# Kernel optimization log

Measured on AMD Instinct MI355X. Metric: run time of the kernel, lower is better.

## Reference

```python
import jax, jax.numpy as jnp
import numpy as np

N_FIL, N_SUB = 13, 4
N_NODES = N_FIL * N_SUB  # 52
FEAT = 6
HID = 128
N_LAYERS = 3
BATCH = 4096


def build_microtubule_edges(nf=N_FIL, ns=N_SUB):
    edges = []
    for i in range(nf):
        for j in range(ns - 1):
            a = i * ns + j
            b = a + 1
            edges += [[a, b], [b, a]]
    for i in range(nf):
        for j in range(ns):
            a = i * ns + j
            l = ((i - 1) % nf) * ns + j
            edges += [[a, l], [l, a]]
            r = ((i + 1) % nf) * ns + j
            edges += [[a, r], [r, a]]
    return np.asarray(edges, dtype=np.int64).T  # (2, 286)


def setup_inputs() -> dict:
    key = jax.random.key(0)
    ks = jax.random.split(key, 10)
    inp = {
        "q_current": jax.random.normal(ks[0], (BATCH, N_FIL, N_SUB, FEAT), jnp.float32),
        "W_in": jax.random.normal(ks[1], (HID, FEAT), jnp.float32) * 0.3,
        "b_in": jax.random.normal(ks[2], (HID,), jnp.float32) * 0.02,
        "W_gnn": jax.random.normal(ks[3], (N_LAYERS, HID, HID), jnp.float32) * (1.0 / np.sqrt(HID)),
        "b_gnn": jax.random.normal(ks[4], (N_LAYERS, HID), jnp.float32) * 0.02,
        "W_d1": jax.random.normal(ks[5], (HID, HID), jnp.float32) * (1.0 / np.sqrt(HID)),
        "b_d1": jax.random.normal(ks[6], (HID,), jnp.float32) * 0.02,
        "W_d2": jax.random.normal(ks[7], (FEAT, HID), jnp.float32) * (1.0 / np.sqrt(HID)),
        "b_d2": jax.random.normal(ks[8], (FEAT,), jnp.float32) * 0.02,
        "edge_index": jnp.asarray(build_microtubule_edges()),
    }
    return inp


def reference(q_current, W_in, b_in, W_gnn, b_gnn, W_d1, b_d1, W_d2, b_d2, edge_index):
    B = q_current.shape[0]
    x0 = q_current.reshape(B, N_NODES, FEAT)

    # PyG GCNConv default: add self-loops, symmetric normalization.
    loops = jnp.arange(N_NODES, dtype=edge_index.dtype)
    src = jnp.concatenate([edge_index[0], loops])  # message source j
    dst = jnp.concatenate([edge_index[1], loops])  # aggregation target i
    deg = jax.ops.segment_sum(jnp.ones_like(dst, dtype=x0.dtype), dst,
                              num_segments=N_NODES)
    dinv = jax.lax.rsqrt(deg)  # deg >= 1 because of self-loops
    norm = (dinv[src] * dinv[dst])[None, :, None]  # (1, E, 1)

    # encoder (batched over B and nodes)
    x = jax.nn.relu(jnp.einsum('bnf,hf->bnh', x0, W_in) + b_in)

    for l in range(N_LAYERS):
        h = jnp.einsum('bnh,oh->bno', x, W_gnn[l])     # linear, no bias
        msg = h[:, src, :] * norm                      # gather + scale
        agg = jnp.zeros_like(h).at[:, dst, :].add(msg)  # scatter-add
        x = x + jax.nn.relu(agg + b_gnn[l])            # bias after agg, residual

    # decoder (Dropout is identity in eval)
    y = jax.nn.relu(jnp.einsum('bnh,oh->bno', x, W_d1) + b_d1)
    y = jnp.einsum('bnh,fh->bnf', y, W_d2) + b_d2
    return y.reshape(B, N_FIL, N_SUB, FEAT)
```

## Files before the change

kernel.cpp:

```cpp
#include <hip/hip_runtime.h>


typedef __attribute__((ext_vector_type(2)))  float  f32x2;
typedef __attribute__((ext_vector_type(4)))  float  f32x4;
typedef __attribute__((ext_vector_type(16))) float  f32x16;
typedef __attribute__((ext_vector_type(8)))  __bf16 bf16x8;

#define MFMA(a, b, c) __builtin_amdgcn_mfma_f32_32x32x16_bf16((a), (b), (c), 0, 0, 0)

__device__ __forceinline__ int xidx(int row, int kdw) {
    return row * 128 + (kdw ^ ((row & 7) << 2));
}

struct bfpair { __bf16 h, l; };
__device__ __forceinline__ bfpair splitf(float f) {
    bfpair p;
    p.h = (__bf16)f;
    p.l = (__bf16)(f - (float)p.h);
    return p;
}

__global__ __launch_bounds__(256) void prep_w(
    const float* __restrict__ Wg, const float* __restrict__ Wd1,
    __bf16* __restrict__ ws)
{
    const int tid  = blockIdx.x * 256 + threadIdx.x;
    const int lane = tid & 31;
    const int hi   = (tid >> 5) & 1;
    const int ot   = (tid >> 6) & 3;
    const int kc   = (tid >> 8) & 7;
    const int L    = tid >> 11;
    const float* src = ((L < 3) ? (Wg + L * 16384) : Wd1)
                     + (ot * 32 + lane) * 128 + kc * 16 + hi * 8;
    const f32x4 v0 = *(const f32x4*)(src);
    const f32x4 v1 = *(const f32x4*)(src + 4);
    bf16x8 h8, l8;
    #pragma unroll
    for (int e = 0; e < 4; ++e) {
        bfpair p0 = splitf(v0[e]); h8[e]   = p0.h; l8[e]   = p0.l;
        bfpair p1 = splitf(v1[e]); h8[4+e] = p1.h; l8[4+e] = p1.l;
    }
    ((bf16x8*)ws)[tid]        = h8;
    ((bf16x8*)ws)[8192 + tid] = l8;
}

__global__ __launch_bounds__(128, 3) void mt_fwd(
    const float* __restrict__ q,   const float* __restrict__ Win, const float* __restrict__ bin,
    const float* __restrict__ bg,  const float* __restrict__ bd1,
    const float* __restrict__ Wd2, const float* __restrict__ bd2,
    const bf16x8* __restrict__ Ph, float* __restrict__ out)
{
    __shared__ __attribute__((aligned(16))) float xs[52 * 128];

    const int t    = threadIdx.x;
    const int nt   = t >> 6;
    const int l    = t & 63;
    const int lane = l & 31;
    const int hi   = l >> 5;
    const int n    = nt * 32 + lane;
    const int nc   = (n < 52) ? n : 0;
    const int samp = blockIdx.x;
    const bf16x8* Pl = Ph + 8192;

    int nb[5]; float nw[5];
    {
        const int   fi = n >> 2, js = n & 3;
        const float dg = 5.f + (js > 0 ? 1.f : 0.f) + (js < 3 ? 1.f : 0.f);
        const float di = rsqrtf(dg);
        nb[0] = n;                          nw[0] = di * di;
        nb[1] = ((fi + 12) % 13) * 4 + js;  nw[1] = 2.f * di * di;
        nb[2] = ((fi + 1) % 13) * 4 + js;   nw[2] = 2.f * di * di;
        nb[3] = (js > 0) ? (n - 1) : 0;
        nw[3] = (js > 0) ? di * rsqrtf(6.f + (js > 1 ? 1.f : 0.f)) : 0.f;
        nb[4] = (js < 3) ? (n + 1) : 0;
        nw[4] = (js < 3) ? di * rsqrtf(6.f + (js < 2 ? 1.f : 0.f)) : 0.f;
        if (n >= 52) {
            #pragma unroll
            for (int c = 0; c < 5; ++c) { nb[c] = 0; nw[c] = 0.f; }
        }
    }

    {
        f32x4 z4; z4[0]=0.f; z4[1]=0.f; z4[2]=0.f; z4[3]=0.f;
        f32x4 u0 = z4, u1 = z4;
        if (hi == 0 && n < 52) {
            const float* qp = q + (samp * 52 + n) * 6;
            const f32x2 a = *(const f32x2*)(qp);
            const f32x2 b = *(const f32x2*)(qp + 2);
            const f32x2 c = *(const f32x2*)(qp + 4);
            u0[0]=a[0]; u0[1]=a[1]; u0[2]=b[0]; u0[3]=b[1]; u1[0]=c[0]; u1[1]=c[1];
        }
        bf16x8 bh, bl;
        #pragma unroll
        for (int e = 0; e < 4; ++e) {
            bfpair p0 = splitf(u0[e]); bh[e]   = p0.h; bl[e]   = p0.l;
            bfpair p1 = splitf(u1[e]); bh[4+e] = p1.h; bl[4+e] = p1.l;
        }

        #pragma unroll
        for (int ot = 0; ot < 4; ++ot) {
            f32x4 v0 = z4, v1 = z4;
            if (hi == 0) {
                const int o_r = ot * 32 + lane;
                const f32x2 a = *(const f32x2*)(Win + o_r * 6);
                const f32x2 b = *(const f32x2*)(Win + o_r * 6 + 2);
                const f32x2 c = *(const f32x2*)(Win + o_r * 6 + 4);
                v0[0]=a[0]; v0[1]=a[1]; v0[2]=b[0]; v0[3]=b[1]; v1[0]=c[0]; v1[1]=c[1];
            }
            bf16x8 ah, al;
            #pragma unroll
            for (int e = 0; e < 4; ++e) {
                bfpair p0 = splitf(v0[e]); ah[e]   = p0.h; al[e]   = p0.l;
                bfpair p1 = splitf(v1[e]); ah[4+e] = p1.h; al[4+e] = p1.l;
            }
            f32x16 acc;
            #pragma unroll
            for (int r = 0; r < 16; ++r) acc[r] = 0.f;
            acc = MFMA(ah, bh, acc);
            acc = MFMA(ah, bl, acc);
            acc = MFMA(al, bh, acc);
            if (n < 52) {
                #pragma unroll
                for (int j = 0; j < 4; ++j) {
                    const f32x4 bv = *(const f32x4*)(bin + ot * 32 + 8 * j + 4 * hi);
                    f32x4 v;
                    #pragma unroll
                    for (int e = 0; e < 4; ++e) v[e] = fmaxf(acc[4 * j + e] + bv[e], 0.f);
                    *(f32x4*)&xs[xidx(n, ot * 32 + 8 * j + 4 * hi)] = v;
                }
            }
        }
    }

    #pragma unroll 1
    for (int L = 0; L < 4; ++L) {
        __syncthreads();

        f32x16 acc[4];
        #pragma unroll
        for (int ot = 0; ot < 4; ++ot)
            #pragma unroll
            for (int r = 0; r < 16; ++r) acc[ot][r] = 0.f;

        const int fbase = (L * 8) * 256;

        #pragma unroll 1
        for (int kc = 0; kc < 8; ++kc) {
            const int kb = kc * 16 + 8 * hi;
            f32x4 a0, a1;
            if (L < 3) {
                #pragma unroll
                for (int e = 0; e < 4; ++e) { a0[e] = 0.f; a1[e] = 0.f; }
                #pragma unroll
                for (int c = 0; c < 5; ++c) {
                    const f32x4 x0 = *(const f32x4*)&xs[xidx(nb[c], kb)];
                    const f32x4 x1 = *(const f32x4*)&xs[xidx(nb[c], kb + 4)];
                    a0 += nw[c] * x0;
                    a1 += nw[c] * x1;
                }
            } else {
                a0 = *(const f32x4*)&xs[xidx(nc, kb)];
                a1 = *(const f32x4*)&xs[xidx(nc, kb + 4)];
            }
            bf16x8 bh, bl;
            #pragma unroll
            for (int e = 0; e < 4; ++e) {
                bfpair p0 = splitf(a0[e]); bh[e]   = p0.h; bl[e]   = p0.l;
                bfpair p1 = splitf(a1[e]); bh[4+e] = p1.h; bl[4+e] = p1.l;
            }

            const int fk = fbase + kc * 256 + hi * 32 + lane;
            #pragma unroll
            for (int ot = 0; ot < 4; ++ot) {
                const bf16x8 wh = Ph[fk + ot * 64];
                const bf16x8 wl = Pl[fk + ot * 64];
                acc[ot] = MFMA(wh, bh, acc[ot]);
                acc[ot] = MFMA(wh, bl, acc[ot]);
                acc[ot] = MFMA(wl, bh, acc[ot]);
            }
        }

        __syncthreads();

        const float* bsrc = (L < 3) ? (bg + L * 128) : bd1;
        if (n < 52) {
            #pragma unroll
            for (int ot = 0; ot < 4; ++ot)
                #pragma unroll
                for (int j = 0; j < 4; ++j) {
                    float* p = &xs[xidx(n, ot * 32 + 8 * j + 4 * hi)];
                    const f32x4 bv = *(const f32x4*)(bsrc + ot * 32 + 8 * j + 4 * hi);
                    f32x4 v;
                    if (L < 3) {
                        const f32x4 cur = *(const f32x4*)p;
                        #pragma unroll
                        for (int e = 0; e < 4; ++e)
                            v[e] = cur[e] + fmaxf(acc[ot][4 * j + e] + bv[e], 0.f);
                    } else {
                        #pragma unroll
                        for (int e = 0; e < 4; ++e)
                            v[e] = fmaxf(acc[ot][4 * j + e] + bv[e], 0.f);
                    }
                    *(f32x4*)p = v;
                }
        }
    }
    __syncthreads();

    {
        f32x16 acc;
        #pragma unroll
        for (int r = 0; r < 16; ++r) acc[r] = 0.f;
        f32x4 z4; z4[0]=0.f; z4[1]=0.f; z4[2]=0.f; z4[3]=0.f;

        #pragma unroll 1
        for (int kc = 0; kc < 8; ++kc) {
            const int kb = kc * 16 + 8 * hi;
            const f32x4 a0 = *(const f32x4*)&xs[xidx(nc, kb)];
            const f32x4 a1 = *(const f32x4*)&xs[xidx(nc, kb + 4)];
            bf16x8 bh, bl;
            #pragma unroll
            for (int e = 0; e < 4; ++e) {
                bfpair p0 = splitf(a0[e]); bh[e]   = p0.h; bl[e]   = p0.l;
                bfpair p1 = splitf(a1[e]); bh[4+e] = p1.h; bl[4+e] = p1.l;
            }
            f32x4 w0 = z4, w1 = z4;
            if (lane < 6) {
                const float* wp = Wd2 + lane * 128 + kb;
                w0 = *(const f32x4*)(wp);
                w1 = *(const f32x4*)(wp + 4);
            }
            bf16x8 ah, al;
            #pragma unroll
            for (int e = 0; e < 4; ++e) {
                bfpair p0 = splitf(w0[e]); ah[e]   = p0.h; al[e]   = p0.l;
                bfpair p1 = splitf(w1[e]); ah[4+e] = p1.h; al[4+e] = p1.l;
            }
            acc = MFMA(ah, bh, acc);
            acc = MFMA(ah, bl, acc);
            acc = MFMA(al, bh, acc);
        }
        if (n < 52) {
            float* op = out + (samp * 52 + n) * 6;
            if (hi == 0) {
                #pragma unroll
                for (int r = 0; r < 4; ++r) op[r] = acc[r] + bd2[r];
            } else {
                #pragma unroll
                for (int r = 0; r < 2; ++r) op[4 + r] = acc[r] + bd2[4 + r];
            }
        }
    }
}

extern "C" void kernel_launch(void* const* d_in, const int* in_sizes, int n_in,
                              void* d_out, int out_size, void* d_ws, size_t ws_size,
                              hipStream_t stream) {
    (void)in_sizes; (void)n_in; (void)ws_size; (void)out_size;
    const float* q   = (const float*)d_in[0];
    const float* Win = (const float*)d_in[1];
    const float* bin = (const float*)d_in[2];
    const float* Wg  = (const float*)d_in[3];
    const float* bg  = (const float*)d_in[4];
    const float* Wd1 = (const float*)d_in[5];
    const float* bd1 = (const float*)d_in[6];
    const float* Wd2 = (const float*)d_in[7];
    const float* bd2 = (const float*)d_in[8];
    float* out = (float*)d_out;

    prep_w<<<32, 256, 0, stream>>>(Wg, Wd1, (__bf16*)d_ws);
    mt_fwd<<<4096, 128, 0, stream>>>(q, Win, bin, bg, bd1, Wd2, bd2,
                                     (const bf16x8*)d_ws, out);
}
```

Before: 157.4 us.

## Reorder GCN layer to transform-then-aggregate with register-resident node features

```diff
diff --git a/kernel.cpp b/kernel.cpp
--- a/kernel.cpp
+++ b/kernel.cpp
@@ -8,9 +8,8 @@
 
 #define MFMA(a, b, c) __builtin_amdgcn_mfma_f32_32x32x16_bf16((a), (b), (c), 0, 0, 0)
 
-__device__ __forceinline__ int xidx(int row, int kdw) {
-    return row * 128 + (kdw ^ ((row & 7) << 2));
-}
+#define QSTR 53
+#define QP   (QSTR * 4)
 
 struct bfpair { __bf16 h, l; };
 __device__ __forceinline__ bfpair splitf(float f) {
@@ -50,7 +49,7 @@
     const float* __restrict__ Wd2, const float* __restrict__ bd2,
     const bf16x8* __restrict__ Ph, float* __restrict__ out)
 {
-    __shared__ __attribute__((aligned(16))) float xs[52 * 128];
+    __shared__ __attribute__((aligned(16))) float hs[32 * QP];
 
     const int t    = threadIdx.x;
     const int nt   = t >> 6;
@@ -61,6 +60,9 @@
     const int nc   = (n < 52) ? n : 0;
     const int samp = blockIdx.x;
     const bf16x8* Pl = Ph + 8192;
+
+    const int wbase = n * 4 + hi * QP;
+    const int rbase = nc * 4 + hi * 2 * QP;
 
     int nb[5]; float nw[5];
     {
@@ -79,6 +81,11 @@
             for (int c = 0; c < 5; ++c) { nb[c] = 0; nw[c] = 0.f; }
         }
     }
+    int gb[5];
+    #pragma unroll
+    for (int c = 0; c < 5; ++c) gb[c] = nb[c] * 4 + hi * 2 * QP;
+
+    bf16x8 bh[8], bl[8];
 
     {
         f32x4 z4; z4[0]=0.f; z4[1]=0.f; z4[2]=0.f; z4[3]=0.f;
@@ -90,11 +97,11 @@
             const f32x2 c = *(const f32x2*)(qp + 4);
             u0[0]=a[0]; u0[1]=a[1]; u0[2]=b[0]; u0[3]=b[1]; u1[0]=c[0]; u1[1]=c[1];
         }
-        bf16x8 bh, bl;
+        bf16x8 qh, ql;
         #pragma unroll
         for (int e = 0; e < 4; ++e) {
-            bfpair p0 = splitf(u0[e]); bh[e]   = p0.h; bl[e]   = p0.l;
-            bfpair p1 = splitf(u1[e]); bh[4+e] = p1.h; bl[4+e] = p1.l;
+            bfpair p0 = splitf(u0[e]); qh[e]   = p0.h; ql[e]   = p0.l;
+            bfpair p1 = splitf(u1[e]); qh[4+e] = p1.h; ql[4+e] = p1.l;
         }
 
         #pragma unroll
@@ -116,9 +123,9 @@
             f32x16 acc;
             #pragma unroll
             for (int r = 0; r < 16; ++r) acc[r] = 0.f;
-            acc = MFMA(ah, bh, acc);
-            acc = MFMA(ah, bl, acc);
-            acc = MFMA(al, bh, acc);
+            acc = MFMA(ah, qh, acc);
+            acc = MFMA(ah, ql, acc);
+            acc = MFMA(al, qh, acc);
             if (n < 52) {
                 #pragma unroll
                 for (int j = 0; j < 4; ++j) {
@@ -126,15 +133,27 @@
                     f32x4 v;
                     #pragma unroll
                     for (int e = 0; e < 4; ++e) v[e] = fmaxf(acc[4 * j + e] + bv[e], 0.f);
-                    *(f32x4*)&xs[xidx(n, ot * 32 + 8 * j + 4 * hi)] = v;
-                }
-            }
-        }
-    }
+                    *(f32x4*)&hs[wbase + (ot * 8 + 2 * j) * QP] = v;
+                }
+            }
+        }
+    }
+    __syncthreads();
+    #pragma unroll
+    for (int kc = 0; kc < 8; ++kc) {
+        const f32x4 a0 = *(const f32x4*)&hs[rbase + (kc * 4 + 0) * QP];
+        const f32x4 a1 = *(const f32x4*)&hs[rbase + (kc * 4 + 1) * QP];
+        #pragma unroll
+        for (int e = 0; e < 4; ++e) {
+            bfpair p0 = splitf(a0[e]); bh[kc][e]   = p0.h; bl[kc][e]   = p0.l;
+            bfpair p1 = splitf(a1[e]); bh[kc][4+e] = p1.h; bl[kc][4+e] = p1.l;
+        }
+    }
+    __syncthreads();
 
     #pragma unroll 1
-    for (int L = 0; L < 4; ++L) {
-        __syncthreads();
+    for (int L = 0; L < 3; ++L) {
+        const int fbase = L * 2048 + hi * 32 + lane;
 
         f32x16 acc[4];
         #pragma unroll
@@ -142,70 +161,115 @@
             #pragma unroll
             for (int r = 0; r < 16; ++r) acc[ot][r] = 0.f;
 
-        const int fbase = (L * 8) * 256;
-
-        #pragma unroll 1
-        for (int kc = 0; kc < 8; ++kc) {
-            const int kb = kc * 16 + 8 * hi;
-            f32x4 a0, a1;
-            if (L < 3) {
-                #pragma unroll
-                for (int e = 0; e < 4; ++e) { a0[e] = 0.f; a1[e] = 0.f; }
-                #pragma unroll
-                for (int c = 0; c < 5; ++c) {
-                    const f32x4 x0 = *(const f32x4*)&xs[xidx(nb[c], kb)];
-                    const f32x4 x1 = *(const f32x4*)&xs[xidx(nb[c], kb + 4)];
-                    a0 += nw[c] * x0;
-                    a1 += nw[c] * x1;
-                }
-            } else {
-                a0 = *(const f32x4*)&xs[xidx(nc, kb)];
-                a1 = *(const f32x4*)&xs[xidx(nc, kb + 4)];
-            }
-            bf16x8 bh, bl;
-            #pragma unroll
-            for (int e = 0; e < 4; ++e) {
-                bfpair p0 = splitf(a0[e]); bh[e]   = p0.h; bl[e]   = p0.l;
-                bfpair p1 = splitf(a1[e]); bh[4+e] = p1.h; bl[4+e] = p1.l;
-            }
-
-            const int fk = fbase + kc * 256 + hi * 32 + lane;
+        #pragma unroll
+        for (int kc = 0; kc < 8; ++kc) {
+            const int fk = fbase + kc * 256;
             #pragma unroll
             for (int ot = 0; ot < 4; ++ot) {
                 const bf16x8 wh = Ph[fk + ot * 64];
                 const bf16x8 wl = Pl[fk + ot * 64];
-                acc[ot] = MFMA(wh, bh, acc[ot]);
-                acc[ot] = MFMA(wh, bl, acc[ot]);
-                acc[ot] = MFMA(wl, bh, acc[ot]);
-            }
-        }
-
+                acc[ot] = MFMA(wh, bh[kc], acc[ot]);
+                acc[ot] = MFMA(wh, bl[kc], acc[ot]);
+                acc[ot] = MFMA(wl, bh[kc], acc[ot]);
+            }
+        }
+
+        if (n < 52) {
+            #pragma unroll
+            for (int ot = 0; ot < 4; ++ot)
+                #pragma unroll
+                for (int j = 0; j < 4; ++j) {
+                    f32x4 v = { acc[ot][4*j+0], acc[ot][4*j+1], acc[ot][4*j+2], acc[ot][4*j+3] };
+                    *(f32x4*)&hs[wbase + (ot * 8 + 2 * j) * QP] = v;
+                }
+        }
         __syncthreads();
 
-        const float* bsrc = (L < 3) ? (bg + L * 128) : bd1;
+        f32x4 t0[8], t1[8];
+        #pragma unroll
+        for (int kc = 0; kc < 8; ++kc)
+            #pragma unroll
+            for (int e = 0; e < 4; ++e) { t0[kc][e] = 0.f; t1[kc][e] = 0.f; }
+        #pragma unroll
+        for (int c = 0; c < 5; ++c) {
+            const float w = nw[c];
+            const int   b = gb[c];
+            #pragma unroll
+            for (int kc = 0; kc < 8; ++kc) {
+                const f32x4 r0 = *(const f32x4*)&hs[b + (kc * 4 + 0) * QP];
+                const f32x4 r1 = *(const f32x4*)&hs[b + (kc * 4 + 1) * QP];
+                t0[kc] += w * r0;
+                t1[kc] += w * r1;
+            }
+        }
+        __syncthreads();
+
+        const float* bsrc = bg + L * 128;
+        #pragma unroll
+        for (int kc = 0; kc < 8; ++kc) {
+            const int f0 = kc * 16 + 8 * hi;
+            const f32x4 b0 = *(const f32x4*)(bsrc + f0);
+            const f32x4 b1 = *(const f32x4*)(bsrc + f0 + 4);
+            #pragma unroll
+            for (int e = 0; e < 4; ++e) {
+                {
+                    const float xo = (float)bh[kc][e] + (float)bl[kc][e];
+                    const float xn = xo + fmaxf(t0[kc][e] + b0[e], 0.f);
+                    bfpair p = splitf(xn); bh[kc][e] = p.h; bl[kc][e] = p.l;
+                }
+                {
+                    const float xo = (float)bh[kc][4+e] + (float)bl[kc][4+e];
+                    const float xn = xo + fmaxf(t1[kc][e] + b1[e], 0.f);
+                    bfpair p = splitf(xn); bh[kc][4+e] = p.h; bl[kc][4+e] = p.l;
+                }
+            }
+        }
+    }
+
+    {
+        const int fbase = 3 * 2048 + hi * 32 + lane;
+        f32x16 acc[4];
+        #pragma unroll
+        for (int ot = 0; ot < 4; ++ot)
+            #pragma unroll
+            for (int r = 0; r < 16; ++r) acc[ot][r] = 0.f;
+        #pragma unroll
+        for (int kc = 0; kc < 8; ++kc) {
+            const int fk = fbase + kc * 256;
+            #pragma unroll
+            for (int ot = 0; ot < 4; ++ot) {
+                const bf16x8 wh = Ph[fk + ot * 64];
+                const bf16x8 wl = Pl[fk + ot * 64];
+                acc[ot] = MFMA(wh, bh[kc], acc[ot]);
+                acc[ot] = MFMA(wh, bl[kc], acc[ot]);
+                acc[ot] = MFMA(wl, bh[kc], acc[ot]);
+            }
+        }
+        __syncthreads();
         if (n < 52) {
             #pragma unroll
             for (int ot = 0; ot < 4; ++ot)
                 #pragma unroll
                 for (int j = 0; j < 4; ++j) {
-                    float* p = &xs[xidx(n, ot * 32 + 8 * j + 4 * hi)];
-                    const f32x4 bv = *(const f32x4*)(bsrc + ot * 32 + 8 * j + 4 * hi);
+                    const f32x4 bv = *(const f32x4*)(bd1 + ot * 32 + 8 * j + 4 * hi);
                     f32x4 v;
-                    if (L < 3) {
-                        const f32x4 cur = *(const f32x4*)p;
-                        #pragma unroll
-                        for (int e = 0; e < 4; ++e)
-                            v[e] = cur[e] + fmaxf(acc[ot][4 * j + e] + bv[e], 0.f);
-                    } else {
-                        #pragma unroll
-                        for (int e = 0; e < 4; ++e)
-                            v[e] = fmaxf(acc[ot][4 * j + e] + bv[e], 0.f);
-                    }
-                    *(f32x4*)p = v;
-                }
-        }
-    }
-    __syncthreads();
+                    #pragma unroll
+                    for (int e = 0; e < 4; ++e) v[e] = fmaxf(acc[ot][4 * j + e] + bv[e], 0.f);
+                    *(f32x4*)&hs[wbase + (ot * 8 + 2 * j) * QP] = v;
+                }
+        }
+        __syncthreads();
+        #pragma unroll
+        for (int kc = 0; kc < 8; ++kc) {
+            const f32x4 a0 = *(const f32x4*)&hs[rbase + (kc * 4 + 0) * QP];
+            const f32x4 a1 = *(const f32x4*)&hs[rbase + (kc * 4 + 1) * QP];
+            #pragma unroll
+            for (int e = 0; e < 4; ++e) {
+                bfpair p0 = splitf(a0[e]); bh[kc][e]   = p0.h; bl[kc][e]   = p0.l;
+                bfpair p1 = splitf(a1[e]); bh[kc][4+e] = p1.h; bl[kc][4+e] = p1.l;
+            }
+        }
+    }
 
     {
         f32x16 acc;
@@ -213,17 +277,9 @@
         for (int r = 0; r < 16; ++r) acc[r] = 0.f;
         f32x4 z4; z4[0]=0.f; z4[1]=0.f; z4[2]=0.f; z4[3]=0.f;
 
-        #pragma unroll 1
+        #pragma unroll
         for (int kc = 0; kc < 8; ++kc) {
             const int kb = kc * 16 + 8 * hi;
-            const f32x4 a0 = *(const f32x4*)&xs[xidx(nc, kb)];
-            const f32x4 a1 = *(const f32x4*)&xs[xidx(nc, kb + 4)];
-            bf16x8 bh, bl;
-            #pragma unroll
-            for (int e = 0; e < 4; ++e) {
-                bfpair p0 = splitf(a0[e]); bh[e]   = p0.h; bl[e]   = p0.l;
-                bfpair p1 = splitf(a1[e]); bh[4+e] = p1.h; bl[4+e] = p1.l;
-            }
             f32x4 w0 = z4, w1 = z4;
             if (lane < 6) {
                 const float* wp = Wd2 + lane * 128 + kb;
@@ -236,9 +292,9 @@
                 bfpair p0 = splitf(w0[e]); ah[e]   = p0.h; al[e]   = p0.l;
                 bfpair p1 = splitf(w1[e]); ah[4+e] = p1.h; al[4+e] = p1.l;
             }
-            acc = MFMA(ah, bh, acc);
-            acc = MFMA(ah, bl, acc);
-            acc = MFMA(al, bh, acc);
+            acc = MFMA(ah, bh[kc], acc);
+            acc = MFMA(ah, bl[kc], acc);
+            acc = MFMA(al, bh[kc], acc);
         }
         if (n < 52) {
             float* op = out + (samp * 52 + n) * 6;
```

Measured after the change: 185.2 us. 1.18x slower.
